# Kernel tuning notes

Hardware: AMD Instinct MI355X
Metric: run time of the kernel (lower is better)

Reference implementation:

```python
import jax, jax.numpy as jnp
import numpy as np

N = 50000
E = 800000


def _degrees(src, dst):
    ones = jnp.ones((E,), dtype=jnp.float32)
    indeg = jax.ops.segment_sum(ones, dst, num_segments=N)
    outdeg = jax.ops.segment_sum(ones, src, num_segments=N)
    return indeg, outdeg


def _aggregate(h, src, dst):
    # update_all(copy_src, sum): gather src features, scatter-add to dst
    return jax.ops.segment_sum(h[src], dst, num_segments=N)


def _graph_conv(h, src, dst, innorm, outnorm, W, b):
    h = h * outnorm[:, None]
    h = _aggregate(h, src, dst)
    h = h * innorm[:, None]
    return h @ W + b


def setup_inputs() -> dict:
    key = jax.random.key(0)
    ks = jax.random.split(key, 8)
    d_in, d_hid, d_out = 128, 128, 64
    inp = {
        "features": jax.random.normal(ks[0], (N, d_in), dtype=jnp.float32),
        "src": jax.random.randint(ks[1], (E,), 0, N, dtype=jnp.int32),
        "dst": jax.random.randint(ks[2], (E,), 0, N, dtype=jnp.int32),
        "W0": jax.random.normal(ks[3], (d_in, d_hid), dtype=jnp.float32) / np.sqrt(d_in),
        "b0": jnp.zeros((d_hid,), dtype=jnp.float32),
        "W1": jax.random.normal(ks[4], (d_hid, d_hid), dtype=jnp.float32) / np.sqrt(d_hid),
        "b1": jnp.zeros((d_hid,), dtype=jnp.float32),
        "W2": jax.random.normal(ks[5], (d_hid, d_hid), dtype=jnp.float32) / np.sqrt(d_hid),
        "b2": jnp.zeros((d_hid,), dtype=jnp.float32),
        "W3": jax.random.normal(ks[6], (d_hid, d_out), dtype=jnp.float32) / np.sqrt(d_hid),
        "b3": jnp.zeros((d_out,), dtype=jnp.float32),
    }
    return inp


def reference(features, src, dst, W0, b0, W1, b1, W2, b2, W3, b3):
    indeg, outdeg = _degrees(src, dst)
    innorm = jnp.power(jnp.clip(indeg, 1.0, None), -0.5)
    outnorm = jnp.power(jnp.clip(outdeg, 1.0, None), -0.5)

    # input GraphConv + relu
    h = jax.nn.relu(_graph_conv(features, src, dst, innorm, outnorm, W0, b0))

    # GResConv blocks: graph_res=True, raw_res=True, dropout=0 (identity)
    for (W, b) in ((W1, b1), (W2, b2)):
        res = features * innorm[:, None]          # pre-norm (in-degree)
        res = _aggregate(res, src, dst)
        res = res * innorm[:, None]               # post-norm (in-degree)
        h = jax.nn.relu(_graph_conv(h, src, dst, innorm, outnorm, W, b) + res)

    # output GraphConv (no activation)
    return _graph_conv(h, src, dst, innorm, outnorm, W3, b3)
```

## Files before the change

### kernel.cpp

```cpp
#include <hip/hip_runtime.h>


#define GN 50000
#define GE 800000
#define SCAN_CHUNK 1024
#define DEG_BLOCKS 64
#define DEG_SLICE 12500
#define HALF_NODES 25000
#define HALF_WORDS 12500

typedef __attribute__((ext_vector_type(8))) short bf16x8;
typedef __attribute__((ext_vector_type(4))) float f32x4;

__device__ __forceinline__ float u2f(unsigned int u) { return __uint_as_float(u); }

__device__ __forceinline__ unsigned int bfr(float a) {
  unsigned int u = __float_as_uint(a);
  return (u + 0x7fffu + ((u >> 16) & 1u)) >> 16;
}
__device__ __forceinline__ unsigned int bfpack(float a, float b) {
  return bfr(a) | (bfr(b) << 16);
}
__device__ __forceinline__ void bfunpack8(uint4 u, float* f) {
  f[0] = u2f(u.x << 16); f[1] = u2f(u.x & 0xffff0000u);
  f[2] = u2f(u.y << 16); f[3] = u2f(u.y & 0xffff0000u);
  f[4] = u2f(u.z << 16); f[5] = u2f(u.z & 0xffff0000u);
  f[6] = u2f(u.w << 16); f[7] = u2f(u.w & 0xffff0000u);
}

__global__ __launch_bounds__(512) void degrees_lds_kernel(
    const int* __restrict__ src, const int* __restrict__ dst,
    unsigned int* __restrict__ partials, int E) {
  __shared__ unsigned int hist[HALF_WORDS];
  for (int i = threadIdx.x; i < HALF_WORDS; i += 512) hist[i] = 0u;
  __syncthreads();
  int b    = blockIdx.x & 63;
  int half = (blockIdx.x >> 6) & 1;
  int dir  = blockIdx.x >> 7;
  const int* __restrict__ idx = dir ? src : dst;
  int lo = half * HALF_NODES, hi = lo + HALF_NODES;
  int s = b * DEG_SLICE;
  int e = min(s + DEG_SLICE, E);
  for (int i = s + threadIdx.x; i < e; i += 512) {
    int node = idx[i];
    if (node >= lo && node < hi) {
      int local = node - lo;
      atomicAdd(&hist[local >> 1], 1u << ((local & 1) << 4));
    }
  }
  __syncthreads();
  unsigned int* outp = partials + (((size_t)dir * 2 + half) * DEG_BLOCKS + b) * HALF_WORDS;
  for (int i = threadIdx.x; i < HALF_WORDS; i += 512) outp[i] = hist[i];
}

__global__ void degrees_reduce_kernel(const unsigned int* __restrict__ partials,
                                      int* __restrict__ indeg, float* __restrict__ innorm,
                                      float* __restrict__ outnorm, float2* __restrict__ nrm2,
                                      unsigned int* __restrict__ rel16pk) {
  int g = blockIdx.x * blockDim.x + threadIdx.x;
  if (g >= 2 * HALF_WORDS) return;
  int half = (g >= HALF_WORDS) ? 1 : 0;
  int w = g - half * HALF_WORDS;
  int n0 = half * HALF_NODES + 2 * w;
  unsigned int inLo = 0, inHi = 0, outLo = 0, outHi = 0;
  const unsigned int* pIn  = partials + ((size_t)(0 * 2 + half) * DEG_BLOCKS) * HALF_WORDS + w;
  const unsigned int* pOut = partials + ((size_t)(1 * 2 + half) * DEG_BLOCKS) * HALF_WORDS + w;
#pragma unroll 4
  for (int b = 0; b < DEG_BLOCKS; b++) {
    rel16pk[((size_t)b * GN + n0) >> 1] = inLo | (inHi << 16);
    unsigned int v = pIn[(size_t)b * HALF_WORDS];
    inLo += v & 0xffffu; inHi += v >> 16;
    unsigned int u = pOut[(size_t)b * HALF_WORDS];
    outLo += u & 0xffffu; outHi += u >> 16;
  }
  indeg[n0]     = (int)inLo;
  indeg[n0 + 1] = (int)inHi;
  float i0 = rsqrtf((float)max((int)inLo, 1)),  i1 = rsqrtf((float)max((int)inHi, 1));
  float o0 = rsqrtf((float)max((int)outLo, 1)), o1 = rsqrtf((float)max((int)outHi, 1));
  innorm[n0] = i0; innorm[n0 + 1] = i1;
  outnorm[n0] = o0; outnorm[n0 + 1] = o1;
  nrm2[n0]     = make_float2(o0, i0);
  nrm2[n0 + 1] = make_float2(o1, i1);
}

__global__ __launch_bounds__(256) void scan_blocksums(const int* __restrict__ deg,
                                                      int* __restrict__ bsums, int n) {
  int tid = threadIdx.x;
  int i = blockIdx.x * SCAN_CHUNK + tid * 4;
  int s = 0;
  if (i + 3 < n) {
    int4 v = *(const int4*)(deg + i);
    s = v.x + v.y + v.z + v.w;
  } else {
    for (int j = 0; j < 4; j++) if (i + j < n) s += deg[i + j];
  }
  for (int off = 32; off; off >>= 1) s += __shfl_down(s, off);
  __shared__ int ws[4];
  if ((tid & 63) == 0) ws[tid >> 6] = s;
  __syncthreads();
  if (tid == 0) bsums[blockIdx.x] = ws[0] + ws[1] + ws[2] + ws[3];
}

__global__ void scan_bsums(const int* __restrict__ bsums, int* __restrict__ bpref,
                           int nb, int* __restrict__ offsets, int n) {
  int tid = threadIdx.x;
  int v = (tid < nb) ? bsums[tid] : 0;
  int incl = v;
  for (int off = 1; off < 64; off <<= 1) {
    int t = __shfl_up(incl, off);
    if (tid >= off) incl += t;
  }
  if (tid < nb) bpref[tid] = incl - v;
  if (tid == 63) offsets[n] = incl;
}

__global__ __launch_bounds__(256) void scan_final(const int* __restrict__ deg,
                                                  const int* __restrict__ bpref,
                                                  int* __restrict__ offsets, int n) {
  int tid = threadIdx.x;
  int i = blockIdx.x * SCAN_CHUNK + tid * 4;
  int v[4];
#pragma unroll
  for (int j = 0; j < 4; j++) v[j] = (i + j < n) ? deg[i + j] : 0;
  int tsum = v[0] + v[1] + v[2] + v[3];
  int incl = tsum;
  for (int off = 1; off < 64; off <<= 1) {
    int t = __shfl_up(incl, off);
    if ((tid & 63) >= off) incl += t;
  }
  __shared__ int wsum[4];
  int wid = tid >> 6, lane = tid & 63;
  if (lane == 63) wsum[wid] = incl;
  __syncthreads();
  int wpref = 0;
  for (int w = 0; w < wid; w++) wpref += wsum[w];
  int run = bpref[blockIdx.x] + wpref + incl - tsum;
#pragma unroll
  for (int j = 0; j < 4; j++) {
    if (i + j < n) offsets[i + j] = run;
    run += v[j];
  }
}

__global__ __launch_bounds__(512) void fill_csr_lds_kernel(
    const int* __restrict__ src, const int* __restrict__ dst,
    const int* __restrict__ offsets, const unsigned short* __restrict__ rel16,
    int* __restrict__ csr, int E) {
  __shared__ unsigned int cnt[HALF_WORDS];
  for (int i = threadIdx.x; i < HALF_WORDS; i += 512) cnt[i] = 0u;
  __syncthreads();
  int b    = blockIdx.x & 63;
  int half = blockIdx.x >> 6;
  int lo = half * HALF_NODES, hi = lo + HALF_NODES;
  int s = b * DEG_SLICE;
  int e = min(s + DEG_SLICE, E);
  const unsigned short* relb = rel16 + (size_t)b * GN;
  for (int i = s + threadIdx.x; i < e; i += 512) {
    int d = dst[i];
    if (d >= lo && d < hi) {
      int local = d - lo;
      int sh = (local & 1) << 4;
      unsigned int old = atomicAdd(&cnt[local >> 1], 1u << sh);
      int rank = (int)((old >> sh) & 0xffffu);
      int pos = offsets[d] + (int)relb[d] + rank;
      csr[pos] = src[i];
    }
  }
}

__global__ __launch_bounds__(256) void f32_to_bf16_kernel(const float* __restrict__ in,
                                                          uint4* __restrict__ out, int n8) {
  int t = blockIdx.x * blockDim.x + threadIdx.x;
  if (t >= n8) return;
  const float4* in4 = (const float4*)in;
  float4 f0 = in4[2 * t], f1 = in4[2 * t + 1];
  uint4 o;
  o.x = bfpack(f0.x, f0.y); o.y = bfpack(f0.z, f0.w);
  o.z = bfpack(f1.x, f1.y); o.w = bfpack(f1.z, f1.w);
  out[t] = o;
}

__global__ __launch_bounds__(256) void wconvert_kernel(
    const float* __restrict__ W0, const float* __restrict__ W1,
    const float* __restrict__ W2, const float* __restrict__ W3,
    unsigned short* __restrict__ wt) {
  int e = blockIdx.x * 256 + threadIdx.x;
  if (e >= 3 * 16384 + 8192) return;
  int m, local, N;
  if (e < 49152) { m = e >> 14; local = e & 16383; N = 128; }
  else { m = 3; local = e - 49152; N = 64; }
  const float* W = (m == 0) ? W0 : (m == 1) ? W1 : (m == 2) ? W2 : W3;
  int k = local / N, n = local % N;
  float v = W[k * N + n];
  unsigned int hi = bfr(v);
  float rem = v - u2f(hi << 16);
  unsigned int lo = bfr(rem);
  size_t hibase = (m < 3) ? (size_t)m * 32768 : 98304;
  size_t lobase = hibase + ((m < 3) ? 16384 : 8192);
  wt[hibase + (size_t)n * 128 + k] = (unsigned short)hi;
  wt[lobase + (size_t)n * 128 + k] = (unsigned short)lo;
}

__global__ __launch_bounds__(256) void aggregate128_bf16_kernel(
    const uint4* __restrict__ hq, const float* __restrict__ gscale,
    const float* __restrict__ wscale, const int* __restrict__ offsets,
    const int* __restrict__ csr, uint4* __restrict__ outq, int n) {
  int node = blockIdx.x * 4 + (threadIdx.x >> 6);
  if (node >= n) return;
  int lane = threadIdx.x & 63;
  int c = lane & 15;
  int p = lane >> 4;
  int s = offsets[node], e = offsets[node + 1];
  float acc[8];
#pragma unroll
  for (int j = 0; j < 8; j++) acc[j] = 0.f;
  int i = s + p;
  for (; i + 12 < e; i += 16) {
    int sn[4];
#pragma unroll
    for (int q = 0; q < 4; q++) sn[q] = csr[i + 4 * q];
    uint4 u[4]; float sv[4];
#pragma unroll
    for (int q = 0; q < 4; q++) {
      u[q] = hq[(size_t)sn[q] * 16 + c];
      sv[q] = gscale[sn[q]];
    }
#pragma unroll
    for (int q = 0; q < 4; q++) {
      float f[8]; bfunpack8(u[q], f);
#pragma unroll
      for (int j = 0; j < 8; j++) acc[j] += f[j] * sv[q];
    }
  }
  for (; i + 4 < e; i += 8) {
    int sn0 = csr[i], sn1 = csr[i + 4];
    uint4 u0 = hq[(size_t)sn0 * 16 + c];
    uint4 u1 = hq[(size_t)sn1 * 16 + c];
    float s0 = gscale[sn0], s1 = gscale[sn1];
    float f0[8], f1[8];
    bfunpack8(u0, f0); bfunpack8(u1, f1);
#pragma unroll
    for (int j = 0; j < 8; j++) acc[j] += f0[j] * s0 + f1[j] * s1;
  }
  if (i < e) {
    int sn = csr[i];
    uint4 u = hq[(size_t)sn * 16 + c];
    float sc = gscale[sn];
    float f[8]; bfunpack8(u, f);
#pragma unroll
    for (int j = 0; j < 8; j++) acc[j] += f[j] * sc;
  }
#pragma unroll
  for (int off = 32; off >= 16; off >>= 1)
#pragma unroll
    for (int j = 0; j < 8; j++) acc[j] += __shfl_down(acc[j], off);
  if (lane < 16) {
    float w = wscale[node];
    uint4 q;
    q.x = bfpack(acc[0] * w, acc[1] * w); q.y = bfpack(acc[2] * w, acc[3] * w);
    q.z = bfpack(acc[4] * w, acc[5] * w); q.w = bfpack(acc[6] * w, acc[7] * w);
    outq[(size_t)node * 16 + c] = q;
  }
}

__global__ __launch_bounds__(256) void aggregate_dual_bf16_kernel(
    const uint4* __restrict__ hq, const float2* __restrict__ nrm2,
    const float* __restrict__ wscale, const int* __restrict__ offsets,
    const int* __restrict__ csr, uint4* __restrict__ out1q,
    uint4* __restrict__ out2q, int n) {
  int node = blockIdx.x * 4 + (threadIdx.x >> 6);
  if (node >= n) return;
  int lane = threadIdx.x & 63;
  int c = lane & 15;
  int p = lane >> 4;
  int s = offsets[node], e = offsets[node + 1];
  float a1[8], a2[8];
#pragma unroll
  for (int j = 0; j < 8; j++) { a1[j] = 0.f; a2[j] = 0.f; }
  int i = s + p;
  for (; i + 12 < e; i += 16) {
    int sn[4];
#pragma unroll
    for (int q = 0; q < 4; q++) sn[q] = csr[i + 4 * q];
    uint4 u[4]; float2 g[4];
#pragma unroll
    for (int q = 0; q < 4; q++) {
      u[q] = hq[(size_t)sn[q] * 16 + c];
      g[q] = nrm2[sn[q]];
    }
#pragma unroll
    for (int q = 0; q < 4; q++) {
      float f[8]; bfunpack8(u[q], f);
#pragma unroll
      for (int j = 0; j < 8; j++) {
        a1[j] += f[j] * g[q].x;
        a2[j] += f[j] * g[q].y;
      }
    }
  }
  for (; i + 4 < e; i += 8) {
    int sn0 = csr[i], sn1 = csr[i + 4];
    uint4 u0 = hq[(size_t)sn0 * 16 + c];
    uint4 u1 = hq[(size_t)sn1 * 16 + c];
    float2 ga = nrm2[sn0], gb = nrm2[sn1];
    float f0[8], f1[8];
    bfunpack8(u0, f0); bfunpack8(u1, f1);
#pragma unroll
    for (int j = 0; j < 8; j++) {
      a1[j] += f0[j] * ga.x + f1[j] * gb.x;
      a2[j] += f0[j] * ga.y + f1[j] * gb.y;
    }
  }
  if (i < e) {
    int sn = csr[i];
    uint4 u = hq[(size_t)sn * 16 + c];
    float2 ga = nrm2[sn];
    float f[8]; bfunpack8(u, f);
#pragma unroll
    for (int j = 0; j < 8; j++) { a1[j] += f[j] * ga.x; a2[j] += f[j] * ga.y; }
  }
#pragma unroll
  for (int off = 32; off >= 16; off >>= 1)
#pragma unroll
    for (int j = 0; j < 8; j++) {
      a1[j] += __shfl_down(a1[j], off);
      a2[j] += __shfl_down(a2[j], off);
    }
  if (lane < 16) {
    float w = wscale[node];
    uint4 q1, q2;
    q1.x = bfpack(a1[0] * w, a1[1] * w); q1.y = bfpack(a1[2] * w, a1[3] * w);
    q1.z = bfpack(a1[4] * w, a1[5] * w); q1.w = bfpack(a1[6] * w, a1[7] * w);
    q2.x = bfpack(a2[0] * w, a2[1] * w); q2.y = bfpack(a2[2] * w, a2[3] * w);
    q2.z = bfpack(a2[4] * w, a2[5] * w); q2.w = bfpack(a2[6] * w, a2[7] * w);
    out1q[(size_t)node * 16 + c] = q1;
    out2q[(size_t)node * 16 + c] = q2;
  }
}

__global__ __launch_bounds__(256) void aggregate64_bf16_kernel(
    const uint4* __restrict__ hq, const float* __restrict__ gscale,
    const float* __restrict__ wscale, const float* __restrict__ bias,
    const int* __restrict__ offsets, const int* __restrict__ csr,
    float* __restrict__ out, int n) {
  int node = blockIdx.x * 4 + (threadIdx.x >> 6);
  if (node >= n) return;
  int lane = threadIdx.x & 63;
  int c = lane & 7;
  int p = lane >> 3;
  int s = offsets[node], e = offsets[node + 1];
  float acc[8];
#pragma unroll
  for (int j = 0; j < 8; j++) acc[j] = 0.f;
  int i = s + p;
  for (; i + 8 < e; i += 16) {
    int sn0 = csr[i], sn1 = csr[i + 8];
    uint4 u0 = hq[(size_t)sn0 * 8 + c];
    uint4 u1 = hq[(size_t)sn1 * 8 + c];
    float s0 = gscale[sn0], s1 = gscale[sn1];
    float f0[8], f1[8];
    bfunpack8(u0, f0); bfunpack8(u1, f1);
#pragma unroll
    for (int j = 0; j < 8; j++) acc[j] += f0[j] * s0 + f1[j] * s1;
  }
  if (i < e) {
    int sn = csr[i];
    uint4 u = hq[(size_t)sn * 8 + c];
    float sc = gscale[sn];
    float f[8]; bfunpack8(u, f);
#pragma unroll
    for (int j = 0; j < 8; j++) acc[j] += f[j] * sc;
  }
#pragma unroll
  for (int off = 32; off >= 8; off >>= 1)
#pragma unroll
    for (int j = 0; j < 8; j++) acc[j] += __shfl_down(acc[j], off);
  if (lane < 8) {
    float w = wscale[node];
    const float4* bp = (const float4*)bias;
    float4 b0 = bp[2 * c], b1 = bp[2 * c + 1];
    float4* orow = (float4*)(out + (size_t)node * 64);
    orow[2 * c]     = make_float4(acc[0] * w + b0.x, acc[1] * w + b0.y,
                                  acc[2] * w + b0.z, acc[3] * w + b0.w);
    orow[2 * c + 1] = make_float4(acc[4] * w + b1.x, acc[5] * w + b1.y,
                                  acc[6] * w + b1.z, acc[7] * w + b1.w);
  }
}

template <int NT, bool RELU, bool HAS_BIAS, bool ADD_RES>
__global__ __launch_bounds__(256) void mfma_gemm_kernel(
    const unsigned short* __restrict__ Abf, const unsigned short* __restrict__ Wth,
    const unsigned short* __restrict__ Wtl, const float* __restrict__ bias,
    const unsigned short* __restrict__ resbf, unsigned short* __restrict__ outbf, int M) {
  constexpr int DOUT = NT * 16;
  int wid = threadIdx.x >> 6, lane = threadIdx.x & 63;
  int row0 = (blockIdx.x * 4 + wid) * 32;
  int lr = lane & 15, g = lane >> 4;
  bf16x8 a[2][4];
  bf16x8 zz = {0, 0, 0, 0, 0, 0, 0, 0};
#pragma unroll
  for (int rt = 0; rt < 2; rt++) {
    int r = row0 + rt * 16 + lr;
    if (r < M) {
      const unsigned short* ap = Abf + (size_t)r * 128 + g * 8;
#pragma unroll
      for (int s = 0; s < 4; s++) a[rt][s] = *(const bf16x8*)(ap + s * 32);
    } else {
#pragma unroll
      for (int s = 0; s < 4; s++) a[rt][s] = zz;
    }
  }
#pragma unroll
  for (int ct = 0; ct < NT; ct++) {
    const unsigned short* wph = Wth + (size_t)(ct * 16 + lr) * 128 + g * 8;
    const unsigned short* wpl = Wtl + (size_t)(ct * 16 + lr) * 128 + g * 8;
    bf16x8 wh[4], wl[4];
#pragma unroll
    for (int s = 0; s < 4; s++) {
      wh[s] = *(const bf16x8*)(wph + s * 32);
      wl[s] = *(const bf16x8*)(wpl + s * 32);
    }
    f32x4 acc0 = {0.f, 0.f, 0.f, 0.f}, acc1 = {0.f, 0.f, 0.f, 0.f};
#pragma unroll
    for (int s = 0; s < 4; s++) {
      acc0 = __builtin_amdgcn_mfma_f32_16x16x32_bf16(a[0][s], wh[s], acc0, 0, 0, 0);
      acc0 = __builtin_amdgcn_mfma_f32_16x16x32_bf16(a[0][s], wl[s], acc0, 0, 0, 0);
      acc1 = __builtin_amdgcn_mfma_f32_16x16x32_bf16(a[1][s], wh[s], acc1, 0, 0, 0);
      acc1 = __builtin_amdgcn_mfma_f32_16x16x32_bf16(a[1][s], wl[s], acc1, 0, 0, 0);
    }
    int col = ct * 16 + lr;
    float bv = HAS_BIAS ? bias[col] : 0.f;
#pragma unroll
    for (int rt = 0; rt < 2; rt++) {
      f32x4 acc = rt ? acc1 : acc0;
#pragma unroll
      for (int j = 0; j < 4; j++) {
        int r = row0 + rt * 16 + g * 4 + j;
        if (r < M) {
          float v = acc[j] + bv;
          if (ADD_RES) v += u2f((unsigned int)resbf[(size_t)r * 128 + col] << 16);
          if (RELU) v = fmaxf(v, 0.f);
          outbf[(size_t)r * DOUT + col] = (unsigned short)bfr(v);
        }
      }
    }
  }
}

extern "C" void kernel_launch(void* const* d_in, const int* in_sizes, int n_in,
                              void* d_out, int out_size, void* d_ws, size_t ws_size,
                              hipStream_t stream) {
  const float* features = (const float*)d_in[0];
  const int*   src      = (const int*)d_in[1];
  const int*   dst      = (const int*)d_in[2];
  const float* W0 = (const float*)d_in[3];
  const float* b0 = (const float*)d_in[4];
  const float* W1 = (const float*)d_in[5];
  const float* b1 = (const float*)d_in[6];
  const float* W2 = (const float*)d_in[7];
  const float* b2 = (const float*)d_in[8];
  const float* W3 = (const float*)d_in[9];
  const float* b3 = (const float*)d_in[10];
  float* out = (float*)d_out;
  const int N = GN, E = GE;

  char* ws = (char*)d_ws;
  size_t off = 0;
  auto alloc = [&](size_t bytes) -> void* {
    void* p = ws + off;
    off = (off + bytes + 255) & ~(size_t)255;
    return p;
  };
  unsigned int* partials = (unsigned int*)alloc((size_t)2 * 2 * DEG_BLOCKS * HALF_WORDS * 4);
  unsigned int* rel16pk  = (unsigned int*)alloc((size_t)DEG_BLOCKS * GN * 2);
  int*   indeg   = (int*)alloc((size_t)N * 4);
  float* innorm  = (float*)alloc((size_t)N * 4);
  float* outnorm = (float*)alloc((size_t)N * 4);
  float2* nrm2   = (float2*)alloc((size_t)N * 8);
  int*   offsets = (int*)alloc((size_t)(N + 1) * 4);
  int*   csr     = (int*)alloc((size_t)E * 4);
  int*   bsums   = (int*)alloc((size_t)256 * 4);
  int*   bpref   = (int*)alloc((size_t)256 * 4);
  unsigned short* wt = (unsigned short*)alloc((size_t)114688 * 2);
  uint4* fbf = (uint4*)alloc((size_t)N * 128 * 2);
  unsigned short* resbf = (unsigned short*)alloc((size_t)N * 128 * 2);
  unsigned short* tbf = (unsigned short*)alloc((size_t)N * 128 * 2);
  unsigned short* hbf = (unsigned short*)alloc((size_t)N * 128 * 2);
  (void)ws_size; (void)in_sizes; (void)n_in; (void)out_size;

  unsigned short* Ybf = resbf;
  const unsigned short *w0h = wt,          *w0l = wt + 16384;
  const unsigned short *w1h = wt + 32768,  *w1l = wt + 49152;
  const unsigned short *w2h = wt + 65536,  *w2l = wt + 81920;
  const unsigned short *w3h = wt + 98304,  *w3l = wt + 106496;

  degrees_lds_kernel<<<256, 512, 0, stream>>>(src, dst, partials, E);
  degrees_reduce_kernel<<<(2 * HALF_WORDS + 255) / 256, 256, 0, stream>>>(
      partials, indeg, innorm, outnorm, nrm2, rel16pk);

  int nb = (N + SCAN_CHUNK - 1) / SCAN_CHUNK;
  scan_blocksums<<<nb, 256, 0, stream>>>(indeg, bsums, N);
  scan_bsums<<<1, 64, 0, stream>>>(bsums, bpref, nb, offsets, N);
  scan_final<<<nb, 256, 0, stream>>>(indeg, bpref, offsets, N);

  fill_csr_lds_kernel<<<128, 512, 0, stream>>>(
      src, dst, offsets, (const unsigned short*)rel16pk, csr, E);

  wconvert_kernel<<<(57344 + 255) / 256, 256, 0, stream>>>(W0, W1, W2, W3, wt);
  f32_to_bf16_kernel<<<(N * 128 / 8 + 255) / 256, 256, 0, stream>>>(
      features, fbf, N * 128 / 8);

  int aggGrid  = (N + 3) / 4;
  int gemmGrid = (N + 127) / 128;

  aggregate_dual_bf16_kernel<<<aggGrid, 256, 0, stream>>>(
      fbf, nrm2, innorm, offsets, csr, (uint4*)tbf, (uint4*)resbf, N);
  mfma_gemm_kernel<8, true, true, false><<<gemmGrid, 256, 0, stream>>>(
      tbf, w0h, w0l, b0, nullptr, hbf, N);
  aggregate128_bf16_kernel<<<aggGrid, 256, 0, stream>>>(
      (const uint4*)hbf, outnorm, innorm, offsets, csr, (uint4*)tbf, N);
  mfma_gemm_kernel<8, true, true, true><<<gemmGrid, 256, 0, stream>>>(
      tbf, w1h, w1l, b1, resbf, hbf, N);
  aggregate128_bf16_kernel<<<aggGrid, 256, 0, stream>>>(
      (const uint4*)hbf, outnorm, innorm, offsets, csr, (uint4*)tbf, N);
  mfma_gemm_kernel<8, true, true, true><<<gemmGrid, 256, 0, stream>>>(
      tbf, w2h, w2l, b2, resbf, hbf, N);
  mfma_gemm_kernel<4, false, false, false><<<gemmGrid, 256, 0, stream>>>(
      hbf, w3h, w3l, nullptr, nullptr, Ybf, N);
  aggregate64_bf16_kernel<<<aggGrid, 256, 0, stream>>>(
      (const uint4*)Ybf, outnorm, innorm, b3, offsets, csr, out, N);
}
```

Before: 363.6 us.

## Precompute per-edge norm scales in CSR and simplify aggregation gather loops

While filling the CSR, each edge's source normalisation pair (from nrm2) is written into a new per-edge float2 array. The aggregation kernels then read this array sequentially instead of doing a random gather of the source node's norm. The aggregation kernels also drop their 4-way unrolled loop and compute gather addresses with 32-bit byte offsets. The degree and CSR-fill kernels now use 128 slices instead of 64, so twice as many blocks are launched. The cost is writing an extra 6.4 MB per-edge buffer and a larger degree-partials buffer for the reduce kernel to sum.

```diff
diff --git a/kernel.cpp b/kernel.cpp
--- a/kernel.cpp
+++ b/kernel.cpp
@@ -4,8 +4,8 @@
 #define GN 50000
 #define GE 800000
 #define SCAN_CHUNK 1024
-#define DEG_BLOCKS 64
-#define DEG_SLICE 12500
+#define DEG_BLOCKS 128
+#define DEG_SLICE 6250
 #define HALF_NODES 25000
 #define HALF_WORDS 12500
 
@@ -34,9 +34,9 @@
   __shared__ unsigned int hist[HALF_WORDS];
   for (int i = threadIdx.x; i < HALF_WORDS; i += 512) hist[i] = 0u;
   __syncthreads();
-  int b    = blockIdx.x & 63;
-  int half = (blockIdx.x >> 6) & 1;
-  int dir  = blockIdx.x >> 7;
+  int b    = blockIdx.x & 127;
+  int half = (blockIdx.x >> 7) & 1;
+  int dir  = blockIdx.x >> 8;
   const int* __restrict__ idx = dir ? src : dst;
   int lo = half * HALF_NODES, hi = lo + HALF_NODES;
   int s = b * DEG_SLICE;
@@ -145,12 +145,13 @@
 __global__ __launch_bounds__(512) void fill_csr_lds_kernel(
     const int* __restrict__ src, const int* __restrict__ dst,
     const int* __restrict__ offsets, const unsigned short* __restrict__ rel16,
-    int* __restrict__ csr, int E) {
+    const float2* __restrict__ nrm2, int* __restrict__ csr,
+    float2* __restrict__ esc2, int E) {
   __shared__ unsigned int cnt[HALF_WORDS];
   for (int i = threadIdx.x; i < HALF_WORDS; i += 512) cnt[i] = 0u;
   __syncthreads();
-  int b    = blockIdx.x & 63;
-  int half = blockIdx.x >> 6;
+  int b    = blockIdx.x & 127;
+  int half = blockIdx.x >> 7;
   int lo = half * HALF_NODES, hi = lo + HALF_NODES;
   int s = b * DEG_SLICE;
   int e = min(s + DEG_SLICE, E);
@@ -163,7 +164,9 @@
       unsigned int old = atomicAdd(&cnt[local >> 1], 1u << sh);
       int rank = (int)((old >> sh) & 0xffffu);
       int pos = offsets[d] + (int)relb[d] + rank;
-      csr[pos] = src[i];
+      int sv = src[i];
+      csr[pos] = sv;
+      esc2[pos] = nrm2[sv];
     }
   }
 }
@@ -202,41 +205,24 @@
 }
 
 __global__ __launch_bounds__(256) void aggregate128_bf16_kernel(
-    const uint4* __restrict__ hq, const float* __restrict__ gscale,
+    const char* __restrict__ hqc, const float2* __restrict__ esc2,
     const float* __restrict__ wscale, const int* __restrict__ offsets,
     const int* __restrict__ csr, uint4* __restrict__ outq, int n) {
   int node = blockIdx.x * 4 + (threadIdx.x >> 6);
   if (node >= n) return;
   int lane = threadIdx.x & 63;
-  int c = lane & 15;
+  unsigned cofs = (unsigned)(lane & 15) << 4;
   int p = lane >> 4;
   int s = offsets[node], e = offsets[node + 1];
   float acc[8];
 #pragma unroll
   for (int j = 0; j < 8; j++) acc[j] = 0.f;
   int i = s + p;
-  for (; i + 12 < e; i += 16) {
-    int sn[4];
-#pragma unroll
-    for (int q = 0; q < 4; q++) sn[q] = csr[i + 4 * q];
-    uint4 u[4]; float sv[4];
-#pragma unroll
-    for (int q = 0; q < 4; q++) {
-      u[q] = hq[(size_t)sn[q] * 16 + c];
-      sv[q] = gscale[sn[q]];
-    }
-#pragma unroll
-    for (int q = 0; q < 4; q++) {
-      float f[8]; bfunpack8(u[q], f);
-#pragma unroll
-      for (int j = 0; j < 8; j++) acc[j] += f[j] * sv[q];
-    }
-  }
   for (; i + 4 < e; i += 8) {
     int sn0 = csr[i], sn1 = csr[i + 4];
-    uint4 u0 = hq[(size_t)sn0 * 16 + c];
-    uint4 u1 = hq[(size_t)sn1 * 16 + c];
-    float s0 = gscale[sn0], s1 = gscale[sn1];
+    float s0 = esc2[i].x, s1 = esc2[i + 4].x;
+    uint4 u0 = *(const uint4*)(hqc + (((unsigned)sn0 << 8) + cofs));
+    uint4 u1 = *(const uint4*)(hqc + (((unsigned)sn1 << 8) + cofs));
     float f0[8], f1[8];
     bfunpack8(u0, f0); bfunpack8(u1, f1);
 #pragma unroll
@@ -244,8 +230,8 @@
   }
   if (i < e) {
     int sn = csr[i];
-    uint4 u = hq[(size_t)sn * 16 + c];
-    float sc = gscale[sn];
+    float sc = esc2[i].x;
+    uint4 u = *(const uint4*)(hqc + (((unsigned)sn << 8) + cofs));
     float f[8]; bfunpack8(u, f);
 #pragma unroll
     for (int j = 0; j < 8; j++) acc[j] += f[j] * sc;
@@ -259,65 +245,45 @@
     uint4 q;
     q.x = bfpack(acc[0] * w, acc[1] * w); q.y = bfpack(acc[2] * w, acc[3] * w);
     q.z = bfpack(acc[4] * w, acc[5] * w); q.w = bfpack(acc[6] * w, acc[7] * w);
-    outq[(size_t)node * 16 + c] = q;
+    outq[(size_t)node * 16 + (lane & 15)] = q;
   }
 }
 
 __global__ __launch_bounds__(256) void aggregate_dual_bf16_kernel(
-    const uint4* __restrict__ hq, const float2* __restrict__ nrm2,
+    const char* __restrict__ hqc, const float2* __restrict__ esc2,
     const float* __restrict__ wscale, const int* __restrict__ offsets,
     const int* __restrict__ csr, uint4* __restrict__ out1q,
     uint4* __restrict__ out2q, int n) {
   int node = blockIdx.x * 4 + (threadIdx.x >> 6);
   if (node >= n) return;
   int lane = threadIdx.x & 63;
-  int c = lane & 15;
+  unsigned cofs = (unsigned)(lane & 15) << 4;
   int p = lane >> 4;
   int s = offsets[node], e = offsets[node + 1];
   float a1[8], a2[8];
 #pragma unroll
   for (int j = 0; j < 8; j++) { a1[j] = 0.f; a2[j] = 0.f; }
   int i = s + p;
-  for (; i + 12 < e; i += 16) {
-    int sn[4];
-#pragma unroll
-    for (int q = 0; q < 4; q++) sn[q] = csr[i + 4 * q];
-    uint4 u[4]; float2 g[4];
-#pragma unroll
-    for (int q = 0; q < 4; q++) {
-      u[q] = hq[(size_t)sn[q] * 16 + c];
-      g[q] = nrm2[sn[q]];
-    }
-#pragma unroll
-    for (int q = 0; q < 4; q++) {
-      float f[8]; bfunpack8(u[q], f);
-#pragma unroll
-      for (int j = 0; j < 8; j++) {
-        a1[j] += f[j] * g[q].x;
-        a2[j] += f[j] * g[q].y;
-      }
-    }
-  }
   for (; i + 4 < e; i += 8) {
     int sn0 = csr[i], sn1 = csr[i + 4];
-    uint4 u0 = hq[(size_t)sn0 * 16 + c];
-    uint4 u1 = hq[(size_t)sn1 * 16 + c];
-    float2 ga = nrm2[sn0], gb = nrm2[sn1];
+    float2 g0 = esc2[i], g1 = esc2[i + 4];
+    uint4 u0 = *(const uint4*)(hqc + (((unsigned)sn0 << 8) + cofs));
+    uint4 u1 = *(const uint4*)(hqc + (((unsigned)sn1 << 8) + cofs));
     float f0[8], f1[8];
     bfunpack8(u0, f0); bfunpack8(u1, f1);
 #pragma unroll
     for (int j = 0; j < 8; j++) {
-      a1[j] += f0[j] * ga.x + f1[j] * gb.x;
-      a2[j] += f0[j] * ga.y + f1[j] * gb.y;
+      a1[j] += f0[j] * g0.x + f1[j] * g1.x;
+      a2[j] += f0[j] * g0.y + f1[j] * g1.y;
     }
   }
   if (i < e) {
     int sn = csr[i];
-    uint4 u = hq[(size_t)sn * 16 + c];
-    float2 ga = nrm2[sn];
+    float2 g = esc2[i];
+    uint4 u = *(const uint4*)(hqc + (((unsigned)sn << 8) + cofs));
     float f[8]; bfunpack8(u, f);
 #pragma unroll
-    for (int j = 0; j < 8; j++) { a1[j] += f[j] * ga.x; a2[j] += f[j] * ga.y; }
+    for (int j = 0; j < 8; j++) { a1[j] += f[j] * g.x; a2[j] += f[j] * g.y; }
   }
 #pragma unroll
   for (int off = 32; off >= 16; off >>= 1)
@@ -333,20 +299,20 @@
     q1.z = bfpack(a1[4] * w, a1[5] * w); q1.w = bfpack(a1[6] * w, a1[7] * w);
     q2.x = bfpack(a2[0] * w, a2[1] * w); q2.y = bfpack(a2[2] * w, a2[3] * w);
     q2.z = bfpack(a2[4] * w, a2[5] * w); q2.w = bfpack(a2[6] * w, a2[7] * w);
-    out1q[(size_t)node * 16 + c] = q1;
-    out2q[(size_t)node * 16 + c] = q2;
+    out1q[(size_t)node * 16 + (lane & 15)] = q1;
+    out2q[(size_t)node * 16 + (lane & 15)] = q2;
   }
 }
 
 __global__ __launch_bounds__(256) void aggregate64_bf16_kernel(
-    const uint4* __restrict__ hq, const float* __restrict__ gscale,
+    const char* __restrict__ hqc, const float2* __restrict__ esc2,
     const float* __restrict__ wscale, const float* __restrict__ bias,
     const int* __restrict__ offsets, const int* __restrict__ csr,
     float* __restrict__ out, int n) {
   int node = blockIdx.x * 4 + (threadIdx.x >> 6);
   if (node >= n) return;
   int lane = threadIdx.x & 63;
-  int c = lane & 7;
+  unsigned cofs = (unsigned)(lane & 7) << 4;
   int p = lane >> 3;
   int s = offsets[node], e = offsets[node + 1];
   float acc[8];
@@ -355,9 +321,9 @@
   int i = s + p;
   for (; i + 8 < e; i += 16) {
     int sn0 = csr[i], sn1 = csr[i + 8];
-    uint4 u0 = hq[(size_t)sn0 * 8 + c];
-    uint4 u1 = hq[(size_t)sn1 * 8 + c];
-    float s0 = gscale[sn0], s1 = gscale[sn1];
+    float s0 = esc2[i].x, s1 = esc2[i + 8].x;
+    uint4 u0 = *(const uint4*)(hqc + (((unsigned)sn0 << 7) + cofs));
+    uint4 u1 = *(const uint4*)(hqc + (((unsigned)sn1 << 7) + cofs));
     float f0[8], f1[8];
     bfunpack8(u0, f0); bfunpack8(u1, f1);
 #pragma unroll
@@ -365,8 +331,8 @@
   }
   if (i < e) {
     int sn = csr[i];
-    uint4 u = hq[(size_t)sn * 8 + c];
-    float sc = gscale[sn];
+    float sc = esc2[i].x;
+    uint4 u = *(const uint4*)(hqc + (((unsigned)sn << 7) + cofs));
     float f[8]; bfunpack8(u, f);
 #pragma unroll
     for (int j = 0; j < 8; j++) acc[j] += f[j] * sc;
@@ -376,6 +342,7 @@
 #pragma unroll
     for (int j = 0; j < 8; j++) acc[j] += __shfl_down(acc[j], off);
   if (lane < 8) {
+    int c = lane;
     float w = wscale[node];
     const float4* bp = (const float4*)bias;
     float4 b0 = bp[2 * c], b1 = bp[2 * c + 1];
@@ -479,6 +446,7 @@
   float2* nrm2   = (float2*)alloc((size_t)N * 8);
   int*   offsets = (int*)alloc((size_t)(N + 1) * 4);
   int*   csr     = (int*)alloc((size_t)E * 4);
+  float2* esc2   = (float2*)alloc((size_t)E * 8);
   int*   bsums   = (int*)alloc((size_t)256 * 4);
   int*   bpref   = (int*)alloc((size_t)256 * 4);
   unsigned short* wt = (unsigned short*)alloc((size_t)114688 * 2);
@@ -494,7 +462,7 @@
   const unsigned short *w2h = wt + 65536,  *w2l = wt + 81920;
   const unsigned short *w3h = wt + 98304,  *w3l = wt + 106496;
 
-  degrees_lds_kernel<<<256, 512, 0, stream>>>(src, dst, partials, E);
+  degrees_lds_kernel<<<4 * DEG_BLOCKS, 512, 0, stream>>>(src, dst, partials, E);
   degrees_reduce_kernel<<<(2 * HALF_WORDS + 255) / 256, 256, 0, stream>>>(
       partials, indeg, innorm, outnorm, nrm2, rel16pk);
 
@@ -503,8 +471,8 @@
   scan_bsums<<<1, 64, 0, stream>>>(bsums, bpref, nb, offsets, N);
   scan_final<<<nb, 256, 0, stream>>>(indeg, bpref, offsets, N);
 
-  fill_csr_lds_kernel<<<128, 512, 0, stream>>>(
-      src, dst, offsets, (const unsigned short*)rel16pk, csr, E);
+  fill_csr_lds_kernel<<<2 * DEG_BLOCKS, 512, 0, stream>>>(
+      src, dst, offsets, (const unsigned short*)rel16pk, nrm2, csr, esc2, E);
 
   wconvert_kernel<<<(57344 + 255) / 256, 256, 0, stream>>>(W0, W1, W2, W3, wt);
   f32_to_bf16_kernel<<<(N * 128 / 8 + 255) / 256, 256, 0, stream>>>(
@@ -514,19 +482,19 @@
   int gemmGrid = (N + 127) / 128;
 
   aggregate_dual_bf16_kernel<<<aggGrid, 256, 0, stream>>>(
-      fbf, nrm2, innorm, offsets, csr, (uint4*)tbf, (uint4*)resbf, N);
+      (const char*)fbf, esc2, innorm, offsets, csr, (uint4*)tbf, (uint4*)resbf, N);
   mfma_gemm_kernel<8, true, true, false><<<gemmGrid, 256, 0, stream>>>(
       tbf, w0h, w0l, b0, nullptr, hbf, N);
   aggregate128_bf16_kernel<<<aggGrid, 256, 0, stream>>>(
-      (const uint4*)hbf, outnorm, innorm, offsets, csr, (uint4*)tbf, N);
+      (const char*)hbf, esc2, innorm, offsets, csr, (uint4*)tbf, N);
   mfma_gemm_kernel<8, true, true, true><<<gemmGrid, 256, 0, stream>>>(
       tbf, w1h, w1l, b1, resbf, hbf, N);
   aggregate128_bf16_kernel<<<aggGrid, 256, 0, stream>>>(
-      (const uint4*)hbf, outnorm, innorm, offsets, csr, (uint4*)tbf, N);
+      (const char*)hbf, esc2, innorm, offsets, csr, (uint4*)tbf, N);
   mfma_gemm_kernel<8, true, true, true><<<gemmGrid, 256, 0, stream>>>(
       tbf, w2h, w2l, b2, resbf, hbf, N);
   mfma_gemm_kernel<4, false, false, false><<<gemmGrid, 256, 0, stream>>>(
       hbf, w3h, w3l, nullptr, nullptr, Ybf, N);
   aggregate64_bf16_kernel<<<aggGrid, 256, 0, stream>>>(
-      (const uint4*)Ybf, outnorm, innorm, b3, offsets, csr, out, N);
-}
+      (const char*)Ybf, esc2, innorm, b3, offsets, csr, out, N);
+}
```

Result: slower. 373.8 us (+2.8%).
